# Performance work log

Measured on AMD Instinct MI355X. Metric: run time of the kernel, lower is better.

## Reference

```python
import jax, jax.numpy as jnp
import numpy as np

B, D, N, F, O = 4096, 256, 128, 128, 256


def setup_inputs() -> dict:
    key = jax.random.key(0)
    ks = jax.random.split(key, 6)
    return {
        "x": jax.random.normal(ks[0], (B, D), dtype=jnp.float32),
        "node_weight": jax.random.normal(ks[1], (N, D + F, F), dtype=jnp.float32),  # torch.randn init
        "node_bias": jax.random.normal(ks[2], (N, F), dtype=jnp.float32),
        "attention": jax.random.normal(ks[3], (N, N), dtype=jnp.float32),
        "out_w": jax.random.normal(ks[4], (F, O), dtype=jnp.float32) * 0.05,  # Linear weight (transposed conv.)
        "out_b": jax.random.normal(ks[5], (O,), dtype=jnp.float32) * 0.05,
        "num_iterations": 3,
    }


def reference(x, node_weight, node_bias, attention, out_w, out_b, num_iterations):
    # connections[i, j] = softmax over j of attention row i
    conn = jax.nn.softmax(attention, axis=1)  # [N, N]
    # Split per-node weight: first F rows act on aggregated states, last D rows on x.
    W_s = node_weight[:, :F, :]   # [N, F, F]
    W_x = node_weight[:, F:, :]   # [N, D, F]
    # x contribution is identical every iteration; precompute once.
    xW = jnp.einsum('bd,ndf->nbf', x, W_x) + node_bias[:, None, :]  # [N, B, F]

    states0 = jnp.zeros((N, B, F), dtype=x.dtype)

    def step(states, _):
        agg = jnp.einsum('ij,jbf->ibf', conn, states)            # attention-weighted aggregation
        new = jax.nn.relu(jnp.einsum('nbf,nfg->nbg', agg, W_s) + xW)
        return new, None

    states, _ = jax.lax.scan(step, states0, None, length=num_iterations)
    final_state = states.mean(axis=0)                            # [B, F]
    return final_state @ out_w + out_b                           # [B, O]
```

## Files before the change

### kernel.cpp

```cpp
#include <hip/hip_runtime.h>

#define DEV __device__ __forceinline__

typedef __attribute__((ext_vector_type(8))) short short8;
typedef __attribute__((ext_vector_type(4))) float floatx4;
typedef __attribute__((ext_vector_type(4))) unsigned short ushort4v;
typedef __attribute__((ext_vector_type(8))) unsigned short ushort8v;

#define Bz 4096
#define Dz 256
#define Nz 128
#define Fz 128
#define Oz 256

static constexpr size_t OFF_CONN = 0;
static constexpr size_t OFF_WT   = 65536;
static constexpr size_t SZ_WT    = (size_t)Nz * 128 * 384 * 2;
static constexpr size_t OFF_OWT  = OFF_WT + SZ_WT;
static constexpr size_t OFF_XB   = OFF_OWT + 65536;
static constexpr size_t OFF_FIN  = OFF_XB + (size_t)Bz * Dz * 2;
static constexpr size_t OFF_ST   = OFF_FIN + (size_t)Bz * Fz * 2;

DEV unsigned short f2bf(float x) {
    unsigned u = __float_as_uint(x);
    u = (u + 0x7FFFu + ((u >> 16) & 1u)) >> 16;
    return (unsigned short)u;
}
DEV float bf2f(unsigned short h) {
    return __uint_as_float(((unsigned)h) << 16);
}

typedef const __attribute__((address_space(1))) void cglobal_void;
typedef __attribute__((address_space(3))) void lds_void;

DEV void gld_lds16(const void* g, void* l) {
    __builtin_amdgcn_global_load_lds((cglobal_void*)g, (lds_void*)l, 16, 0, 0);
}

__global__ __launch_bounds__(64) void k_softmax(const float* __restrict__ att,
                                                unsigned short* __restrict__ conn) {
    int i = blockIdx.x, t = threadIdx.x;
    float a0 = att[i * 128 + t];
    float a1 = att[i * 128 + 64 + t];
    float m = fmaxf(a0, a1);
    for (int o = 32; o > 0; o >>= 1) m = fmaxf(m, __shfl_down(m, o));
    m = __shfl(m, 0);
    float e0 = __expf(a0 - m), e1 = __expf(a1 - m);
    float s = e0 + e1;
    for (int o = 32; o > 0; o >>= 1) s += __shfl_down(s, o);
    s = __shfl(s, 0);
    float inv = 1.f / s;
    conn[i * 128 + t] = f2bf(e0 * inv);
    conn[i * 128 + 64 + t] = f2bf(e1 * inv);
}

__global__ __launch_bounds__(256) void k_transpose(const float* __restrict__ src,
                                                   unsigned short* __restrict__ dst,
                                                   int R, int C, int tilesC,
                                                   long sBatch, long dBatch) {
    __shared__ float ld[32][36];
    int tiles = (R / 32) * tilesC;
    int batch = blockIdx.x / tiles;
    int rem = blockIdx.x % tiles;
    int rt = rem / tilesC, ct = rem % tilesC;
    int t = threadIdx.x;
    int kr = t >> 3, c4 = (t & 7) * 4;
    float4 v = *(const float4*)&src[(size_t)batch * sBatch + (size_t)(rt * 32 + kr) * C + ct * 32 + c4];
    ld[kr][c4 + 0] = v.x; ld[kr][c4 + 1] = v.y; ld[kr][c4 + 2] = v.z; ld[kr][c4 + 3] = v.w;
    __syncthreads();
    int cr = kr, k4 = c4;
    ushort4v o;
    o[0] = f2bf(ld[k4 + 0][cr]);
    o[1] = f2bf(ld[k4 + 1][cr]);
    o[2] = f2bf(ld[k4 + 2][cr]);
    o[3] = f2bf(ld[k4 + 3][cr]);
    *(ushort4v*)&dst[(size_t)batch * dBatch + (size_t)(ct * 32 + cr) * R + rt * 32 + k4] = o;
}

__global__ __launch_bounds__(256) void k_convert(const float* __restrict__ src,
                                                 unsigned short* __restrict__ dst) {
    size_t idx = ((size_t)blockIdx.x * 256 + threadIdx.x) * 4;
    float4 v = *(const float4*)&src[idx];
    ushort4v o;
    o[0] = f2bf(v.x); o[1] = f2bf(v.y); o[2] = f2bf(v.z); o[3] = f2bf(v.w);
    *(ushort4v*)&dst[idx] = o;
}

__global__ __launch_bounds__(256) void k2_agg(const unsigned short* __restrict__ conn,
                                              unsigned short* __restrict__ ST) {
    __shared__ unsigned short lA[128 * 136];
    __shared__ unsigned short lB[2][32 * 128];
    int b = blockIdx.x;
    int t = threadIdx.x, wid = t >> 6, lane = t & 63, q = lane >> 4, cc = lane & 15;
    int wm = (wid >> 1) << 6, wn = (wid & 1) << 6;

    auto STG = [&](int bufi, int kt) {
#pragma unroll
        for (int it = 0; it < 2; it++) {
            int g = it * 256 + t;
            int j = g >> 4, fg = g & 15;
            int lofs = __builtin_amdgcn_readfirstlane((it * 256 + (wid << 6)) * 8);
            gld_lds16(ST + ((size_t)(kt * 32 + j) * Bz + b) * Fz + fg * 8, &lB[bufi][0] + lofs);
        }
    };
    STG(0, 0);
    STG(1, 1);

#pragma unroll
    for (int it = 0; it < 8; it++) {
        int g = it * 256 + t;
        int row = g >> 4, cg = g & 15;
        *(short8*)&lA[row * 136 + cg * 8] = *(const short8*)&conn[row * 128 + cg * 8];
    }
    floatx4 acc[4][4];
#pragma unroll
    for (int mt = 0; mt < 4; mt++)
#pragma unroll
        for (int nt = 0; nt < 4; nt++) acc[mt][nt] = (floatx4){0.f, 0.f, 0.f, 0.f};

    for (int kt = 0; kt < 4; kt++) {
        int cur = kt & 1;
        if (kt < 3) asm volatile("s_waitcnt vmcnt(2) lgkmcnt(0)" ::: "memory");
        else        asm volatile("s_waitcnt vmcnt(0) lgkmcnt(0)" ::: "memory");
        __builtin_amdgcn_s_barrier();
        short8 af[4];
#pragma unroll
        for (int mt = 0; mt < 4; mt++)
            af[mt] = *(const short8*)&lA[(wm + mt * 16 + cc) * 136 + kt * 32 + q * 8];
        short8 bf[4];
#pragma unroll
        for (int nt = 0; nt < 4; nt++) {
            short8 v;
#pragma unroll
            for (int e = 0; e < 8; e++)
                v[e] = (short)lB[cur][(q * 8 + e) * 128 + wn + nt * 16 + cc];
            bf[nt] = v;
        }
#pragma unroll
        for (int mt = 0; mt < 4; mt++)
#pragma unroll
            for (int nt = 0; nt < 4; nt++)
                acc[mt][nt] = __builtin_amdgcn_mfma_f32_16x16x32_bf16(af[mt], bf[nt], acc[mt][nt], 0, 0, 0);
        __builtin_amdgcn_s_barrier();
        if (kt + 2 < 4) STG(cur, kt + 2);
    }

#pragma unroll
    for (int mt = 0; mt < 4; mt++)
#pragma unroll
        for (int nt = 0; nt < 4; nt++) {
            int f = wn + nt * 16 + cc;
#pragma unroll
            for (int r = 0; r < 4; r++) {
                int il = wm + mt * 16 + q * 4 + r;
                lA[il * 128 + (f ^ ((il & 7) << 3))] = f2bf(acc[mt][nt][r]);
            }
        }
    __syncthreads();
#pragma unroll
    for (int it = 0; it < 8; it++) {
        int idx = it * 256 + t;
        int il = idx >> 4, ch = idx & 15;
        int sch = ch ^ (il & 7);
        ushort8v v = *(const ushort8v*)&lA[il * 128 + sch * 8];
        *(ushort8v*)&ST[((size_t)il * Bz + b) * Fz + ch * 8] = v;
    }
}

template <int KT0>
__global__ __launch_bounds__(256) void k3_fused(unsigned short* __restrict__ ST,
                                                const unsigned short* __restrict__ XB,
                                                const unsigned short* __restrict__ WT,
                                                const float* __restrict__ nb) {
    __shared__ unsigned short lds[3][2][128 * 32];
    int n = blockIdx.x >> 5, bt = blockIdx.x & 31;
    int t = threadIdx.x, wid = t >> 6, lane = t & 63, q = lane >> 4, cc = lane & 15;
    int wm = (wid >> 1) << 6, wn = (wid & 1) << 6;

    const unsigned short* Sg = ST + ((size_t)n * Bz + bt * 128) * Fz;
    const unsigned short* Xg = XB + (size_t)bt * 128 * Dz;
    const unsigned short* Bg = WT + (size_t)n * 128 * 384;

    floatx4 acc[4][4];
#pragma unroll
    for (int mt = 0; mt < 4; mt++)
#pragma unroll
        for (int nt = 0; nt < 4; nt++) acc[mt][nt] = (floatx4){0.f, 0.f, 0.f, 0.f};

    auto STAGE = [&](int bufi, int kt) {
#pragma unroll
        for (int it = 0; it < 2; it++) {
            int g = it * 256 + t;
            int row = g >> 2, kg = g & 3;
            int lofs = __builtin_amdgcn_readfirstlane((it * 256 + (wid << 6)) * 8);
            if (kt < 4)
                gld_lds16(Sg + (size_t)row * Fz + kt * 32 + kg * 8, &lds[bufi][0][0] + lofs);
            else
                gld_lds16(Xg + (size_t)row * Dz + (kt - 4) * 32 + kg * 8, &lds[bufi][0][0] + lofs);
            gld_lds16(Bg + (size_t)row * 384 + kt * 32 + kg * 8, &lds[bufi][1][0] + lofs);
        }
    };
    STAGE(0, KT0);
    STAGE(1, KT0 + 1);
    STAGE(2, KT0 + 2);

#pragma unroll
    for (int kt = KT0; kt < 12; kt++) {
        int cur = (kt - KT0) % 3;
        if (kt < 10)      asm volatile("s_waitcnt vmcnt(8) lgkmcnt(0)" ::: "memory");
        else if (kt < 11) asm volatile("s_waitcnt vmcnt(4) lgkmcnt(0)" ::: "memory");
        else              asm volatile("s_waitcnt vmcnt(0) lgkmcnt(0)" ::: "memory");
        __builtin_amdgcn_s_barrier();
        __builtin_amdgcn_sched_barrier(0);
        short8 af[4], bfr[4];
#pragma unroll
        for (int mt = 0; mt < 4; mt++)
            af[mt] = *(const short8*)&lds[cur][0][(wm + mt * 16 + cc) * 32 + q * 8];
#pragma unroll
        for (int nt = 0; nt < 4; nt++)
            bfr[nt] = *(const short8*)&lds[cur][1][(wn + nt * 16 + cc) * 32 + q * 8];
#pragma unroll
        for (int mt = 0; mt < 4; mt++)
#pragma unroll
            for (int nt = 0; nt < 4; nt++)
                acc[mt][nt] = __builtin_amdgcn_mfma_f32_16x16x32_bf16(af[mt], bfr[nt], acc[mt][nt], 0, 0, 0);
        __builtin_amdgcn_sched_barrier(0);
        __builtin_amdgcn_s_barrier();
        if (kt + 3 < 12) STAGE(cur, kt + 3);
    }

    unsigned short* outT = &lds[0][0][0];
#pragma unroll
    for (int nt = 0; nt < 4; nt++) {
        int f = wn + nt * 16 + cc;
        float bias = nb[n * Fz + f];
#pragma unroll
        for (int mt = 0; mt < 4; mt++) {
#pragma unroll
            for (int r = 0; r < 4; r++) {
                int bl = wm + mt * 16 + q * 4 + r;
                float v = acc[mt][nt][r] + bias;
                outT[bl * 128 + (f ^ ((bl & 7) << 3))] = f2bf(v > 0.f ? v : 0.f);
            }
        }
    }
    __syncthreads();
    size_t base = ((size_t)n * Bz + (size_t)bt * 128) * Fz;
#pragma unroll
    for (int it = 0; it < 8; it++) {
        int idx = it * 256 + t;
        int bl = idx >> 4, ch = idx & 15;
        int sch = ch ^ (bl & 7);
        ushort8v v = *(const ushort8v*)&outT[bl * 128 + sch * 8];
        *(ushort8v*)&ST[base + (size_t)idx * 8] = v;
    }
}

__global__ __launch_bounds__(256) void k4_mean(const unsigned short* __restrict__ S,
                                               unsigned short* __restrict__ fin) {
    int t = threadIdx.x;
    size_t base = (size_t)blockIdx.x * 2048 + (size_t)t * 8;
    float a[8] = {0.f, 0.f, 0.f, 0.f, 0.f, 0.f, 0.f, 0.f};
#pragma unroll 8
    for (int n = 0; n < Nz; n++) {
        ushort8v v = *(const ushort8v*)&S[(size_t)n * Bz * Fz + base];
#pragma unroll
        for (int e = 0; e < 8; e++) a[e] += bf2f(v[e]);
    }
    ushort8v o;
#pragma unroll
    for (int e = 0; e < 8; e++) o[e] = f2bf(a[e] * (1.f / 128.f));
    *(ushort8v*)&fin[base] = o;
}

__global__ __launch_bounds__(256) void k5_out(const unsigned short* __restrict__ fin,
                                              const unsigned short* __restrict__ owt,
                                              const float* __restrict__ ob,
                                              float* __restrict__ out) {
    __shared__ unsigned short lA[128 * 32];
    __shared__ unsigned short lB[128 * 32];
    int bt = blockIdx.x >> 1, ct = blockIdx.x & 1;
    int t = threadIdx.x, wid = t >> 6, lane = t & 63, q = lane >> 4, cc = lane & 15;
    int wm = (wid >> 1) << 6, wn = (wid & 1) << 6;

    const unsigned short* Ag = fin + (size_t)bt * 128 * Fz;
    const unsigned short* Bg = owt + (size_t)ct * 128 * Fz;

    floatx4 acc[4][4];
#pragma unroll
    for (int mt = 0; mt < 4; mt++)
#pragma unroll
        for (int nt = 0; nt < 4; nt++) acc[mt][nt] = (floatx4){0.f, 0.f, 0.f, 0.f};

    for (int kt = 0; kt < 4; kt++) {
#pragma unroll
        for (int it = 0; it < 2; it++) {
            int g = it * 256 + t;
            int row = g >> 2, kg = g & 3;
            int lofs = __builtin_amdgcn_readfirstlane((it * 256 + (wid << 6)) * 8);
            gld_lds16(Ag + (size_t)row * Fz + kt * 32 + kg * 8, lA + lofs);
            gld_lds16(Bg + (size_t)row * Fz + kt * 32 + kg * 8, lB + lofs);
        }
        __syncthreads();
        short8 af[4], bfr[4];
#pragma unroll
        for (int mt = 0; mt < 4; mt++)
            af[mt] = *(const short8*)&lA[(wm + mt * 16 + cc) * 32 + q * 8];
#pragma unroll
        for (int nt = 0; nt < 4; nt++)
            bfr[nt] = *(const short8*)&lB[(wn + nt * 16 + cc) * 32 + q * 8];
#pragma unroll
        for (int mt = 0; mt < 4; mt++)
#pragma unroll
            for (int nt = 0; nt < 4; nt++)
                acc[mt][nt] = __builtin_amdgcn_mfma_f32_16x16x32_bf16(af[mt], bfr[nt], acc[mt][nt], 0, 0, 0);
        __syncthreads();
    }
#pragma unroll
    for (int nt = 0; nt < 4; nt++) {
        int o = ct * 128 + wn + nt * 16 + cc;
        float bias = ob[o];
#pragma unroll
        for (int mt = 0; mt < 4; mt++) {
#pragma unroll
            for (int r = 0; r < 4; r++) {
                int b = bt * 128 + wm + mt * 16 + q * 4 + r;
                out[(size_t)b * Oz + o] = acc[mt][nt][r] + bias;
            }
        }
    }
}

extern "C" void kernel_launch(void* const* d_in, const int* in_sizes, int n_in,
                              void* d_out, int out_size, void* d_ws, size_t ws_size,
                              hipStream_t stream) {
    const float* x = (const float*)d_in[0];
    const float* nw = (const float*)d_in[1];
    const float* nb = (const float*)d_in[2];
    const float* att = (const float*)d_in[3];
    const float* ow = (const float*)d_in[4];
    const float* ob = (const float*)d_in[5];
    char* ws = (char*)d_ws;
    unsigned short* CONN = (unsigned short*)(ws + OFF_CONN);
    unsigned short* WT = (unsigned short*)(ws + OFF_WT);
    unsigned short* OWT = (unsigned short*)(ws + OFF_OWT);
    unsigned short* XB = (unsigned short*)(ws + OFF_XB);
    unsigned short* FIN = (unsigned short*)(ws + OFF_FIN);
    unsigned short* ST = (unsigned short*)(ws + OFF_ST);
    float* out = (float*)d_out;

    k_softmax<<<Nz, 64, 0, stream>>>(att, CONN);
    k_transpose<<<Nz * 48, 256, 0, stream>>>(nw, WT, 384, 128, 4, (long)384 * 128, (long)128 * 384);
    k_transpose<<<32, 256, 0, stream>>>(ow, OWT, 128, 256, 8, 0, 0);
    k_convert<<<(Bz * Dz) / 1024, 256, 0, stream>>>(x, XB);

    k3_fused<4><<<Nz * 32, 256, 0, stream>>>(ST, XB, WT, nb);

    for (int it = 0; it < 2; it++) {
        k2_agg<<<Bz, 256, 0, stream>>>(CONN, ST);
        k3_fused<0><<<Nz * 32, 256, 0, stream>>>(ST, XB, WT, nb);
    }

    k4_mean<<<(Bz * Fz) / 2048, 256, 0, stream>>>(ST, FIN);
    k5_out<<<64, 256, 0, stream>>>(FIN, OWT, ob, out);
}
```

Before: 399.8 us.

## Fuse node-mean into final layer via atomics and merge prep kernels

Merges the softmax, transpose and convert preprocessing kernels into one launch. The last state-update kernel no longer writes bf16 states; it atomically accumulates the scaled ReLU outputs into an fp32 mean buffer, removing the separate mean kernel and the final state write and read. The output GEMM converts the fp32 mean to bf16 on load. In exchange it issues tens of millions of contended fp32 atomics and gives a nondeterministic summation order.

```diff
diff --git a/kernel.cpp b/kernel.cpp
--- a/kernel.cpp
+++ b/kernel.cpp
@@ -20,6 +20,7 @@
 static constexpr size_t OFF_XB   = OFF_OWT + 65536;
 static constexpr size_t OFF_FIN  = OFF_XB + (size_t)Bz * Dz * 2;
 static constexpr size_t OFF_ST   = OFF_FIN + (size_t)Bz * Fz * 2;
+static constexpr size_t OFF_F32  = OFF_ST + (size_t)Nz * Bz * Fz * 2;
 
 DEV unsigned short f2bf(float x) {
     unsigned u = __float_as_uint(x);
@@ -37,53 +38,59 @@
     __builtin_amdgcn_global_load_lds((cglobal_void*)g, (lds_void*)l, 16, 0, 0);
 }
 
-__global__ __launch_bounds__(64) void k_softmax(const float* __restrict__ att,
-                                                unsigned short* __restrict__ conn) {
-    int i = blockIdx.x, t = threadIdx.x;
-    float a0 = att[i * 128 + t];
-    float a1 = att[i * 128 + 64 + t];
-    float m = fmaxf(a0, a1);
-    for (int o = 32; o > 0; o >>= 1) m = fmaxf(m, __shfl_down(m, o));
-    m = __shfl(m, 0);
-    float e0 = __expf(a0 - m), e1 = __expf(a1 - m);
-    float s = e0 + e1;
-    for (int o = 32; o > 0; o >>= 1) s += __shfl_down(s, o);
-    s = __shfl(s, 0);
-    float inv = 1.f / s;
-    conn[i * 128 + t] = f2bf(e0 * inv);
-    conn[i * 128 + 64 + t] = f2bf(e1 * inv);
-}
-
-__global__ __launch_bounds__(256) void k_transpose(const float* __restrict__ src,
-                                                   unsigned short* __restrict__ dst,
-                                                   int R, int C, int tilesC,
-                                                   long sBatch, long dBatch) {
+__global__ __launch_bounds__(256) void k_prep(const float* __restrict__ nw, unsigned short* __restrict__ WT,
+                                              const float* __restrict__ ow, unsigned short* __restrict__ OWT,
+                                              const float* __restrict__ x, unsigned short* __restrict__ XB,
+                                              const float* __restrict__ att, unsigned short* __restrict__ conn) {
     __shared__ float ld[32][36];
-    int tiles = (R / 32) * tilesC;
-    int batch = blockIdx.x / tiles;
-    int rem = blockIdx.x % tiles;
-    int rt = rem / tilesC, ct = rem % tilesC;
-    int t = threadIdx.x;
-    int kr = t >> 3, c4 = (t & 7) * 4;
-    float4 v = *(const float4*)&src[(size_t)batch * sBatch + (size_t)(rt * 32 + kr) * C + ct * 32 + c4];
-    ld[kr][c4 + 0] = v.x; ld[kr][c4 + 1] = v.y; ld[kr][c4 + 2] = v.z; ld[kr][c4 + 3] = v.w;
-    __syncthreads();
-    int cr = kr, k4 = c4;
-    ushort4v o;
-    o[0] = f2bf(ld[k4 + 0][cr]);
-    o[1] = f2bf(ld[k4 + 1][cr]);
-    o[2] = f2bf(ld[k4 + 2][cr]);
-    o[3] = f2bf(ld[k4 + 3][cr]);
-    *(ushort4v*)&dst[(size_t)batch * dBatch + (size_t)(ct * 32 + cr) * R + rt * 32 + k4] = o;
-}
-
-__global__ __launch_bounds__(256) void k_convert(const float* __restrict__ src,
-                                                 unsigned short* __restrict__ dst) {
-    size_t idx = ((size_t)blockIdx.x * 256 + threadIdx.x) * 4;
-    float4 v = *(const float4*)&src[idx];
-    ushort4v o;
-    o[0] = f2bf(v.x); o[1] = f2bf(v.y); o[2] = f2bf(v.z); o[3] = f2bf(v.w);
-    *(ushort4v*)&dst[idx] = o;
+    int bid = blockIdx.x, t = threadIdx.x;
+    if (bid < 6144) {
+        int batch = bid / 48, rem = bid % 48;
+        int rt = rem / 4, ct = rem % 4;
+        int kr = t >> 3, c4 = (t & 7) * 4;
+        float4 v = *(const float4*)&nw[(size_t)batch * (384 * 128) + (size_t)(rt * 32 + kr) * 128 + ct * 32 + c4];
+        ld[kr][c4 + 0] = v.x; ld[kr][c4 + 1] = v.y; ld[kr][c4 + 2] = v.z; ld[kr][c4 + 3] = v.w;
+        __syncthreads();
+        ushort4v o;
+        o[0] = f2bf(ld[c4 + 0][kr]);
+        o[1] = f2bf(ld[c4 + 1][kr]);
+        o[2] = f2bf(ld[c4 + 2][kr]);
+        o[3] = f2bf(ld[c4 + 3][kr]);
+        *(ushort4v*)&WT[(size_t)batch * (128 * 384) + (size_t)(ct * 32 + kr) * 384 + rt * 32 + c4] = o;
+    } else if (bid < 6176) {
+        int rem = bid - 6144;
+        int rt = rem / 8, ct = rem % 8;
+        int kr = t >> 3, c4 = (t & 7) * 4;
+        float4 v = *(const float4*)&ow[(size_t)(rt * 32 + kr) * 256 + ct * 32 + c4];
+        ld[kr][c4 + 0] = v.x; ld[kr][c4 + 1] = v.y; ld[kr][c4 + 2] = v.z; ld[kr][c4 + 3] = v.w;
+        __syncthreads();
+        ushort4v o;
+        o[0] = f2bf(ld[c4 + 0][kr]);
+        o[1] = f2bf(ld[c4 + 1][kr]);
+        o[2] = f2bf(ld[c4 + 2][kr]);
+        o[3] = f2bf(ld[c4 + 3][kr]);
+        *(ushort4v*)&OWT[(size_t)(ct * 32 + kr) * 128 + rt * 32 + c4] = o;
+    } else if (bid < 7200) {
+        size_t idx = ((size_t)(bid - 6176) * 256 + t) * 4;
+        float4 v = *(const float4*)&x[idx];
+        ushort4v o;
+        o[0] = f2bf(v.x); o[1] = f2bf(v.y); o[2] = f2bf(v.z); o[3] = f2bf(v.w);
+        *(ushort4v*)&XB[idx] = o;
+    } else if (t < 64) {
+        int i = bid - 7200;
+        float a0 = att[i * 128 + t];
+        float a1 = att[i * 128 + 64 + t];
+        float m = fmaxf(a0, a1);
+        for (int o = 32; o > 0; o >>= 1) m = fmaxf(m, __shfl_down(m, o));
+        m = __shfl(m, 0);
+        float e0 = __expf(a0 - m), e1 = __expf(a1 - m);
+        float s = e0 + e1;
+        for (int o = 32; o > 0; o >>= 1) s += __shfl_down(s, o);
+        s = __shfl(s, 0);
+        float inv = 1.f / s;
+        conn[i * 128 + t] = f2bf(e0 * inv);
+        conn[i * 128 + 64 + t] = f2bf(e1 * inv);
+    }
 }
 
 __global__ __launch_bounds__(256) void k2_agg(const unsigned short* __restrict__ conn,
@@ -167,11 +174,12 @@
     }
 }
 
-template <int KT0>
+template <int KT0, int MEAN>
 __global__ __launch_bounds__(256) void k3_fused(unsigned short* __restrict__ ST,
                                                 const unsigned short* __restrict__ XB,
                                                 const unsigned short* __restrict__ WT,
-                                                const float* __restrict__ nb) {
+                                                const float* __restrict__ nb,
+                                                float* __restrict__ fin32) {
     __shared__ unsigned short lds[3][2][128 * 32];
     int n = blockIdx.x >> 5, bt = blockIdx.x & 31;
     int t = threadIdx.x, wid = t >> 6, lane = t & 63, q = lane >> 4, cc = lane & 15;
@@ -229,51 +237,53 @@
         if (kt + 3 < 12) STAGE(cur, kt + 3);
     }
 
-    unsigned short* outT = &lds[0][0][0];
-#pragma unroll
-    for (int nt = 0; nt < 4; nt++) {
-        int f = wn + nt * 16 + cc;
-        float bias = nb[n * Fz + f];
-#pragma unroll
-        for (int mt = 0; mt < 4; mt++) {
-#pragma unroll
-            for (int r = 0; r < 4; r++) {
-                int bl = wm + mt * 16 + q * 4 + r;
-                float v = acc[mt][nt][r] + bias;
-                outT[bl * 128 + (f ^ ((bl & 7) << 3))] = f2bf(v > 0.f ? v : 0.f);
+    if (MEAN == 0) {
+        unsigned short* outT = &lds[0][0][0];
+#pragma unroll
+        for (int nt = 0; nt < 4; nt++) {
+            int f = wn + nt * 16 + cc;
+            float bias = nb[n * Fz + f];
+#pragma unroll
+            for (int mt = 0; mt < 4; mt++) {
+#pragma unroll
+                for (int r = 0; r < 4; r++) {
+                    int bl = wm + mt * 16 + q * 4 + r;
+                    float v = acc[mt][nt][r] + bias;
+                    outT[bl * 128 + (f ^ ((bl & 7) << 3))] = f2bf(v > 0.f ? v : 0.f);
+                }
             }
         }
-    }
-    __syncthreads();
-    size_t base = ((size_t)n * Bz + (size_t)bt * 128) * Fz;
-#pragma unroll
-    for (int it = 0; it < 8; it++) {
-        int idx = it * 256 + t;
-        int bl = idx >> 4, ch = idx & 15;
-        int sch = ch ^ (bl & 7);
-        ushort8v v = *(const ushort8v*)&outT[bl * 128 + sch * 8];
-        *(ushort8v*)&ST[base + (size_t)idx * 8] = v;
-    }
-}
-
-__global__ __launch_bounds__(256) void k4_mean(const unsigned short* __restrict__ S,
-                                               unsigned short* __restrict__ fin) {
-    int t = threadIdx.x;
-    size_t base = (size_t)blockIdx.x * 2048 + (size_t)t * 8;
-    float a[8] = {0.f, 0.f, 0.f, 0.f, 0.f, 0.f, 0.f, 0.f};
-#pragma unroll 8
-    for (int n = 0; n < Nz; n++) {
-        ushort8v v = *(const ushort8v*)&S[(size_t)n * Bz * Fz + base];
-#pragma unroll
-        for (int e = 0; e < 8; e++) a[e] += bf2f(v[e]);
-    }
-    ushort8v o;
-#pragma unroll
-    for (int e = 0; e < 8; e++) o[e] = f2bf(a[e] * (1.f / 128.f));
-    *(ushort8v*)&fin[base] = o;
-}
-
-__global__ __launch_bounds__(256) void k5_out(const unsigned short* __restrict__ fin,
+        __syncthreads();
+        size_t base = ((size_t)n * Bz + (size_t)bt * 128) * Fz;
+#pragma unroll
+        for (int it = 0; it < 8; it++) {
+            int idx = it * 256 + t;
+            int bl = idx >> 4, ch = idx & 15;
+            int sch = ch ^ (bl & 7);
+            ushort8v v = *(const ushort8v*)&outT[bl * 128 + sch * 8];
+            *(ushort8v*)&ST[base + (size_t)idx * 8] = v;
+        }
+    } else {
+        const float sc = 1.f / 128.f;
+#pragma unroll
+        for (int nt = 0; nt < 4; nt++) {
+            int f = wn + nt * 16 + cc;
+            float bias = nb[n * Fz + f];
+#pragma unroll
+            for (int mt = 0; mt < 4; mt++) {
+#pragma unroll
+                for (int r = 0; r < 4; r++) {
+                    int bl = wm + mt * 16 + q * 4 + r;
+                    float v = acc[mt][nt][r] + bias;
+                    v = v > 0.f ? v : 0.f;
+                    atomicAdd(&fin32[(size_t)(bt * 128 + bl) * Fz + f], v * sc);
+                }
+            }
+        }
+    }
+}
+
+__global__ __launch_bounds__(256) void k5_out(const float* __restrict__ fin32,
                                               const unsigned short* __restrict__ owt,
                                               const float* __restrict__ ob,
                                               float* __restrict__ out) {
@@ -283,7 +293,7 @@
     int t = threadIdx.x, wid = t >> 6, lane = t & 63, q = lane >> 4, cc = lane & 15;
     int wm = (wid >> 1) << 6, wn = (wid & 1) << 6;
 
-    const unsigned short* Ag = fin + (size_t)bt * 128 * Fz;
+    const float* Ag = fin32 + (size_t)bt * 128 * Fz;
     const unsigned short* Bg = owt + (size_t)ct * 128 * Fz;
 
     floatx4 acc[4][4];
@@ -293,12 +303,20 @@
         for (int nt = 0; nt < 4; nt++) acc[mt][nt] = (floatx4){0.f, 0.f, 0.f, 0.f};
 
     for (int kt = 0; kt < 4; kt++) {
+#pragma unroll
+        for (int it = 0; it < 4; it++) {
+            int g = it * 256 + t;
+            int row = g >> 3, c4 = (g & 7) * 4;
+            float4 v = *(const float4*)&Ag[(size_t)row * Fz + kt * 32 + c4];
+            ushort4v o;
+            o[0] = f2bf(v.x); o[1] = f2bf(v.y); o[2] = f2bf(v.z); o[3] = f2bf(v.w);
+            *(ushort4v*)&lA[row * 32 + c4] = o;
+        }
 #pragma unroll
         for (int it = 0; it < 2; it++) {
             int g = it * 256 + t;
             int row = g >> 2, kg = g & 3;
             int lofs = __builtin_amdgcn_readfirstlane((it * 256 + (wid << 6)) * 8);
-            gld_lds16(Ag + (size_t)row * Fz + kt * 32 + kg * 8, lA + lofs);
             gld_lds16(Bg + (size_t)row * Fz + kt * 32 + kg * 8, lB + lofs);
         }
         __syncthreads();
@@ -345,22 +363,20 @@
     unsigned short* WT = (unsigned short*)(ws + OFF_WT);
     unsigned short* OWT = (unsigned short*)(ws + OFF_OWT);
     unsigned short* XB = (unsigned short*)(ws + OFF_XB);
-    unsigned short* FIN = (unsigned short*)(ws + OFF_FIN);
     unsigned short* ST = (unsigned short*)(ws + OFF_ST);
+    float* FIN32 = (float*)(ws + OFF_F32);
     float* out = (float*)d_out;
 
-    k_softmax<<<Nz, 64, 0, stream>>>(att, CONN);
-    k_transpose<<<Nz * 48, 256, 0, stream>>>(nw, WT, 384, 128, 4, (long)384 * 128, (long)128 * 384);
-    k_transpose<<<32, 256, 0, stream>>>(ow, OWT, 128, 256, 8, 0, 0);
-    k_convert<<<(Bz * Dz) / 1024, 256, 0, stream>>>(x, XB);
-
-    k3_fused<4><<<Nz * 32, 256, 0, stream>>>(ST, XB, WT, nb);
-
-    for (int it = 0; it < 2; it++) {
-        k2_agg<<<Bz, 256, 0, stream>>>(CONN, ST);
-        k3_fused<0><<<Nz * 32, 256, 0, stream>>>(ST, XB, WT, nb);
-    }
-
-    k4_mean<<<(Bz * Fz) / 2048, 256, 0, stream>>>(ST, FIN);
-    k5_out<<<64, 256, 0, stream>>>(FIN, OWT, ob, out);
-}
+    k_prep<<<7328, 256, 0, stream>>>(nw, WT, ow, OWT, x, XB, att, CONN);
+
+    k3_fused<4, 0><<<Nz * 32, 256, 0, stream>>>(ST, XB, WT, nb, nullptr);
+
+    k2_agg<<<Bz, 256, 0, stream>>>(CONN, ST);
+    k3_fused<0, 0><<<Nz * 32, 256, 0, stream>>>(ST, XB, WT, nb, nullptr);
+
+    k2_agg<<<Bz, 256, 0, stream>>>(CONN, ST);
+    hipMemsetAsync(FIN32, 0, (size_t)Bz * Fz * 4, stream);
+    k3_fused<0, 1><<<Nz * 32, 256, 0, stream>>>(ST, XB, WT, nb, FIN32);
+
+    k5_out<<<64, 256, 0, stream>>>(FIN32, OWT, ob, out);
+}
```

Result: slower. 515.1 us (+28.8%).
